# Kernel tuning notes

Hardware: AMD Instinct MI355X
Metric: run time of the kernel (lower is better)

## Reference

```python
import jax, jax.numpy as jnp
import numpy as np

EPS = 1e-08
N_NODES = 100000
D = 128
N_EDGES = 3200000


def _gcn_conv(x, w, b, edge_index, n):
    # PyG GCNConv: add self-loops, symmetric deg^{-1/2} normalization,
    # out = scatter_add(norm * (x @ w)[src] -> dst) + bias
    loops = jnp.arange(n, dtype=edge_index.dtype)
    src = jnp.concatenate([edge_index[0], loops])
    dst = jnp.concatenate([edge_index[1], loops])
    deg = jax.ops.segment_sum(jnp.ones_like(dst, dtype=x.dtype), dst, num_segments=n)
    dinv = jnp.where(deg > 0, jax.lax.rsqrt(deg), 0.0)
    norm = dinv[src] * dinv[dst]                      # [E+N]
    h = x @ w                                          # [N, D]
    msg = h[src] * norm[:, None]                       # [E+N, D] (dominant traffic)
    return jax.ops.segment_sum(msg, dst, num_segments=n) + b


def setup_inputs() -> dict:
    key = jax.random.key(0)
    ks = jax.random.split(key, 8)
    s = 1.0 / np.sqrt(D)
    return {
        "edge_index": jax.random.randint(ks[0], (2, N_EDGES), 0, N_NODES, dtype=jnp.int64),
        "eps": jax.random.normal(ks[1], (N_NODES, D), dtype=jnp.float32),
        "vrepr": jax.random.normal(ks[2], (N_NODES, D), dtype=jnp.float32) * 0.02,
        "conv_w": jax.random.uniform(ks[3], (D, D), jnp.float32, -s, s),
        "conv_b": jnp.zeros((D,), jnp.float32),
        "loc_w": jax.random.uniform(ks[4], (D, D), jnp.float32, -s, s),
        "loc_b": jax.random.uniform(ks[5], (D,), jnp.float32, -s, s),
        "std_w": jax.random.uniform(ks[6], (D, D), jnp.float32, -s, s),
        "std_b": jax.random.uniform(ks[7], (D,), jnp.float32, -s, s),
    }


def reference(edge_index, eps, vrepr, conv_w, conv_b, loc_w, loc_b, std_w, std_b):
    n = vrepr.shape[0]
    h = _gcn_conv(vrepr, conv_w, conv_b, edge_index, n)   # [N, D]
    loc = h @ loc_w.T + loc_b
    std = jax.nn.softplus(h @ std_w.T + std_b) + EPS
    logvar = jnp.log(std ** 2)
    z = loc + std * eps                                    # Normal(loc, std).rsample()
    return (z, loc, logvar)
```

## Files before the change

### kernel.cpp

```cpp
#include <hip/hip_runtime.h>
#include <math.h>


typedef short short8 __attribute__((ext_vector_type(8)));
typedef float f32x4 __attribute__((ext_vector_type(4)));

#define NT 64
#define MAXCELL 1568
#define CPT 7
#define CHUNK 8192
#define CHUNKC 32768
#define CAPB 4096
#define BPB 256
#define RPT (CAPB / BPB)
#define FBLK 768

static __device__ __forceinline__ unsigned short f2bf(float x) {
  unsigned u = __float_as_uint(x);
  unsigned r = (u + 0x7fffu + ((u >> 16) & 1u)) >> 16;
  return (unsigned short)r;
}


#if __has_builtin(__builtin_amdgcn_cvt_f32_fp8)
static __device__ __forceinline__ float fp8dec(unsigned v, int sel) {
  switch (sel) {
    case 0: return __builtin_amdgcn_cvt_f32_fp8((int)v, 0);
    case 1: return __builtin_amdgcn_cvt_f32_fp8((int)v, 1);
    case 2: return __builtin_amdgcn_cvt_f32_fp8((int)v, 2);
    default: return __builtin_amdgcn_cvt_f32_fp8((int)v, 3);
  }
}
#else
static __device__ __forceinline__ float fp8dec1(unsigned b) {
  unsigned s = b >> 7, e = (b >> 3) & 15, m = b & 7;
  float mag = e ? __uint_as_float(((e + 120u) << 23) | (m << 20))
                : (float)m * 0.001953125f;
  return s ? -mag : mag;
}
static __device__ __forceinline__ float fp8dec(unsigned v, int sel) {
  return fp8dec1((v >> (8 * sel)) & 0xff);
}
#endif

static __device__ __forceinline__ unsigned fp8enc(float v) {
#if __has_builtin(__builtin_amdgcn_cvt_pk_fp8_f32)
  return (unsigned)__builtin_amdgcn_cvt_pk_fp8_f32(v, 0.0f, 0, false) & 0xffu;
#else
  unsigned u = __float_as_uint(v);
  unsigned s = (u >> 24) & 0x80u;
  int e = (int)((u >> 23) & 0xff) - 127;
  unsigned m = u & 0x7fffffu;
  if (e < -9) return s;
  if (e >= 9) return s | 0x7e;
  if (e >= -6) {
    unsigned keep = m >> 20;
    unsigned rem = m & 0xfffffu;
    keep += (rem > 0x80000u) || (rem == 0x80000u && (keep & 1));
    unsigned ee = (unsigned)(e + 7);
    if (keep == 8) { keep = 0; ee += 1; if (ee >= 16) return s | 0x7e; }
    return s | (ee << 3) | keep;
  }
  float q = fabsf(v) * 512.0f;
  unsigned k = (unsigned)(q + 0.5f);
  if (k >= 8) return s | 0x08;
  return s | k;
#endif
}

static __device__ void block_scan_cells(int* cnt, int* off, int* scanT, int ncell, int tid)
{
  int c0 = tid * CPT;
  int lsum = 0;
#pragma unroll
  for (int u = 0; u < CPT; ++u) { int c = c0 + u; if (c < ncell) lsum += cnt[c]; }
  scanT[tid] = lsum;
  __syncthreads();
  for (int o = 1; o < 256; o <<= 1) {
    int add = (tid >= o) ? scanT[tid - o] : 0;
    __syncthreads();
    scanT[tid] += add;
    __syncthreads();
  }
  int run = scanT[tid] - lsum;
#pragma unroll
  for (int u = 0; u < CPT; ++u) {
    int c = c0 + u;
    if (c < ncell) { off[c] = run; run += cnt[c]; }
  }
}

__global__ void k_zero_int(int* __restrict__ p, int n) {
  int i = blockIdx.x * blockDim.x + threadIdx.x;
  if (i < n) p[i] = 0;
}


__global__ __launch_bounds__(512)
void k_cellcnt(const int4* __restrict__ dst4, int* __restrict__ cellCnt, int nE4, int ncell)
{
  __shared__ int h[MAXCELL];
  const int tid = threadIdx.x;
  const int base4 = blockIdx.x * (CHUNKC / 4);
  for (int i = tid; i < ncell; i += 512) h[i] = 0;
  __syncthreads();
#pragma unroll
  for (int k = 0; k < CHUNKC / 4 / 512; ++k) {
    int i4 = base4 + tid + k * 512;
    if (i4 < nE4) {
      int4 d = dst4[i4];
      atomicAdd(&h[d.x >> 6], 1);
      atomicAdd(&h[d.y >> 6], 1);
      atomicAdd(&h[d.z >> 6], 1);
      atomicAdd(&h[d.w >> 6], 1);
    }
  }
  __syncthreads();
  for (int i = tid; i < ncell; i += 512) if (h[i]) atomicAdd(&cellCnt[i], h[i]);
}


__global__ __launch_bounds__(256)
void k_cellscan(const int* __restrict__ cellCnt, int* __restrict__ gOff,
                int* __restrict__ gCur, int ncell)
{
  __shared__ int c[MAXCELL], o[MAXCELL], scanT[256];
  const int tid = threadIdx.x;
  for (int i = tid; i < ncell; i += 256) c[i] = cellCnt[i];
  __syncthreads();
  block_scan_cells(c, o, scanT, ncell, tid);
  __syncthreads();
  for (int i = tid; i < ncell; i += 256) { gOff[i] = o[i]; gCur[i] = o[i]; }
}


__global__ __launch_bounds__(256)
void k_passA(const int4* __restrict__ src4, const int4* __restrict__ dst4,
             int* __restrict__ gCur, unsigned* __restrict__ gEdges, int nE4, int ncell)
{
  __shared__ unsigned stagePk[CHUNK];
  __shared__ unsigned short stageCell[CHUNK];
  __shared__ int cntA[MAXCELL], offA[MAXCELL], curA[MAXCELL], scanT[256];
  const int tid = threadIdx.x;
  const int base4 = blockIdx.x * (CHUNK / 4);
  const int C = min(CHUNK, nE4 * 4 - base4 * 4);

  for (int i = tid; i < ncell; i += 256) cntA[i] = 0;
  __syncthreads();
#pragma unroll
  for (int k = 0; k < CHUNK / 4 / 256; ++k) {
    int i4 = base4 + tid + k * 256;
    if (i4 < nE4) {
      int4 d = dst4[i4];
      atomicAdd(&cntA[d.x >> 6], 1);
      atomicAdd(&cntA[d.y >> 6], 1);
      atomicAdd(&cntA[d.z >> 6], 1);
      atomicAdd(&cntA[d.w >> 6], 1);
    }
  }
  __syncthreads();
  block_scan_cells(cntA, offA, scanT, ncell, tid);
  __syncthreads();
  for (int i = tid; i < ncell; i += 256) curA[i] = offA[i];
  __syncthreads();
#pragma unroll
  for (int k = 0; k < CHUNK / 4 / 256; ++k) {
    int i4 = base4 + tid + k * 256;
    if (i4 < nE4) {
      int4 d = dst4[i4];
      int4 s = src4[i4];
#pragma unroll
      for (int u = 0; u < 4; ++u) {
        int dd = (u == 0) ? d.x : (u == 1) ? d.y : (u == 2) ? d.z : d.w;
        int ss = (u == 0) ? s.x : (u == 1) ? s.y : (u == 2) ? s.z : s.w;
        int c = dd >> 6, dl = dd & 63;
        int pos = atomicAdd(&curA[c], 1);
        stagePk[pos] = (unsigned)ss | ((unsigned)dl << 17);
        stageCell[pos] = (unsigned short)c;
      }
    }
  }
  __syncthreads();
  for (int i = tid; i < ncell; i += 256) {
    int cv = cntA[i];
    if (cv > 0) {
      int b = atomicAdd(&gCur[i], cv);
      cntA[i] = b - offA[i];
    }
  }
  __syncthreads();
#pragma unroll
  for (int k = 0; k < CHUNK / 256; ++k) {
    int p = tid + k * 256;
    if (p < C) {
      int c = stageCell[p];
      gEdges[cntA[c] + p] = stagePk[p];
    }
  }
}


__global__ __launch_bounds__(256)
void k_cnt_dinv(const unsigned* __restrict__ gEdges, const int* __restrict__ gOff,
                const int* __restrict__ cellCnt, float* __restrict__ dinv, int n)
{
  __shared__ int cnt[NT];
  const int c = blockIdx.x, tid = threadIdx.x;
  if (tid < NT) cnt[tid] = 0;
  __syncthreads();
  const int off = gOff[c], m = cellCnt[c];
  for (int i = tid; i < m; i += 256) atomicAdd(&cnt[gEdges[off + i] >> 17], 1);
  __syncthreads();
  int d = c * NT + tid;
  if (tid < NT && d < n) dinv[d] = rsqrtf((float)cnt[tid] + 1.0f);
}


__global__ void k_vs(const float* __restrict__ vrepr, const float* __restrict__ dinv,
                     unsigned* __restrict__ vs, int n)
{
  int i = blockIdx.x * 256 + threadIdx.x;
  if (i >= n * 32) return;
  int row = i >> 5;
  float4 v = ((const float4*)vrepr)[i];
  float dd = dinv[row] * 128.0f;
#if __has_builtin(__builtin_amdgcn_cvt_pk_fp8_f32)
  int w = __builtin_amdgcn_cvt_pk_fp8_f32(v.x * dd, v.y * dd, 0, false);
  w = __builtin_amdgcn_cvt_pk_fp8_f32(v.z * dd, v.w * dd, w, true);
  vs[i] = (unsigned)w;
#else
  vs[i] = fp8enc(v.x * dd) | (fp8enc(v.y * dd) << 8) |
          (fp8enc(v.z * dd) << 16) | (fp8enc(v.w * dd) << 24);
#endif
}


__global__ __launch_bounds__(128)
void k_wcomb(const float* __restrict__ cw, const float* __restrict__ cb,
             const float* __restrict__ hw, const float* __restrict__ hb,
             unsigned short* __restrict__ wt, float* __restrict__ bout)
{
  int j = blockIdx.x, k = threadIdx.x;
  __shared__ float s[128];
  s[k] = hw[j * 128 + k];
  __syncthreads();
  float acc = 0.f;
  const float* r = cw + k * 128;
#pragma unroll 8
  for (int m = 0; m < 128; ++m) acc = fmaf(r[m], s[m], acc);
  wt[j * 128 + k] = f2bf(acc);
  if (k == 0) {
    float b = 0.f;
    for (int m = 0; m < 128; ++m) b = fmaf(cb[m], s[m], b);
    bout[j] = b + hb[j];
  }
}


__global__ __launch_bounds__(BPB)
void k_passB(const unsigned* __restrict__ gEdges, const int* __restrict__ gOff,
             const int* __restrict__ cellCnt, const float* __restrict__ dinv,
             const unsigned* __restrict__ vs32, float* __restrict__ hagg, int n)
{
  __shared__ unsigned sortedE[CAPB];
  __shared__ int hist[NT];
  __shared__ int segOff[NT + 1];
  const int c = blockIdx.x, tid = threadIdx.x;
  const int d0 = c * NT;
  const int off0 = gOff[c], m = cellCnt[c];
  const int wv = tid >> 6, lane = tid & 63;
  const int half = lane >> 5;
  const int l32 = lane & 31;

  const int nchunk = m > 0 ? (m + CAPB - 1) / CAPB : 1;
  for (int ch = 0; ch < nchunk; ++ch) {
    const int cb = ch * CAPB;
    const int mc = min(CAPB, m - cb) > 0 ? min(CAPB, m - cb) : 0;

    if (ch > 0) __syncthreads();
    for (int i = tid; i < NT; i += BPB) hist[i] = 0;
    __syncthreads();

    unsigned rawE[RPT];
#pragma unroll
    for (int k = 0; k < RPT; ++k) {
      int i = tid + k * BPB;
      unsigned pk = 0xffffffffu;
      if (i < mc) {
        pk = gEdges[off0 + cb + i];
        atomicAdd(&hist[pk >> 17], 1);
      }
      rawE[k] = pk;
    }
    __syncthreads();
    if (tid == 0) {
      int run = 0;
      for (int r = 0; r < NT; ++r) { segOff[r] = run; run += hist[r]; }
      segOff[NT] = run;
    }
    __syncthreads();
    for (int i = tid; i < NT; i += BPB) hist[i] = segOff[i];
    __syncthreads();
#pragma unroll
    for (int k = 0; k < RPT; ++k) {
      unsigned pk = rawE[k];
      if (pk != 0xffffffffu)
        sortedE[atomicAdd(&hist[pk >> 17], 1)] = pk;
    }
    __syncthreads();

    for (int r = wv; r < NT; r += 4) {
      int d = d0 + r;
      if (d >= n) continue;
      float a0 = 0.f, a1 = 0.f, a2 = 0.f, a3 = 0.f;
      int i = segOff[r];
      const int e = segOff[r + 1];
      for (; i + 16 <= e; i += 16) {
#pragma unroll
        for (int j = 0; j < 8; ++j) {
          unsigned pk = sortedE[i + 2 * j + half];
          unsigned v = vs32[(size_t)(pk & 0x1FFFF) * 32 + l32];
          a0 += fp8dec(v, 0); a1 += fp8dec(v, 1);
          a2 += fp8dec(v, 2); a3 += fp8dec(v, 3);
        }
      }
      for (; i + 2 <= e; i += 2) {
        unsigned pk = sortedE[i + half];
        unsigned v = vs32[(size_t)(pk & 0x1FFFF) * 32 + l32];
        a0 += fp8dec(v, 0); a1 += fp8dec(v, 1);
        a2 += fp8dec(v, 2); a3 += fp8dec(v, 3);
      }
      if (i < e && half == 0) {
        unsigned pk = sortedE[i];
        unsigned v = vs32[(size_t)(pk & 0x1FFFF) * 32 + l32];
        a0 += fp8dec(v, 0); a1 += fp8dec(v, 1);
        a2 += fp8dec(v, 2); a3 += fp8dec(v, 3);
      }
      a0 += __shfl_xor(a0, 32);
      a1 += __shfl_xor(a1, 32);
      a2 += __shfl_xor(a2, 32);
      a3 += __shfl_xor(a3, 32);

      if (half == 0) {
        const float dd = dinv[d] * 0.0078125f;
        float4 out;
        if (ch == 0) {
          unsigned sp = vs32[(size_t)d * 32 + l32];
          out = make_float4((a0 + fp8dec(sp, 0)) * dd, (a1 + fp8dec(sp, 1)) * dd,
                            (a2 + fp8dec(sp, 2)) * dd, (a3 + fp8dec(sp, 3)) * dd);
        } else {
          float4 prev = ((const float4*)hagg)[(size_t)d * 32 + l32];
          out = make_float4(prev.x + a0 * dd, prev.y + a1 * dd,
                            prev.z + a2 * dd, prev.w + a3 * dd);
        }
        ((float4*)hagg)[(size_t)d * 32 + l32] = out;
      }
    }
  }
}


#define LPAD 132

__global__ __launch_bounds__(512)
void k_fused(const float* hagg,
             const unsigned short* __restrict__ wlT, const unsigned short* __restrict__ wsT,
             const float* __restrict__ bl, const float* __restrict__ bs,
             const float* __restrict__ eps,
             float* __restrict__ z, float* loc, float* __restrict__ lv,
             int n, int ntiles)
{
  __shared__ float sLoc[32 * LPAD];
  __shared__ float sStd[32 * LPAD];
  const int t = threadIdx.x;
  const int w = t >> 6;
  const int L = t & 63;
  const int rg = (w >> 2) * 16;
  const int c0 = (w & 3) * 32;
  const int lr = L & 15;
  const int lk = L >> 4;

  short8 bw[2][2][4];
  float blv[2], bsv[2];
#pragma unroll
  for (int head = 0; head < 2; ++head) {
    const unsigned short* W = head ? wsT : wlT;
#pragma unroll
    for (int ct = 0; ct < 2; ++ct) {
      int col = c0 + ct * 16 + lr;
#pragma unroll
      for (int kt = 0; kt < 4; ++kt)
        bw[head][ct][kt] = *(const short8*)(W + col * 128 + kt * 32 + lk * 8);
    }
  }
#pragma unroll
  for (int ct = 0; ct < 2; ++ct) {
    blv[ct] = bl[c0 + ct * 16 + lr];
    bsv[ct] = bs[c0 + ct * 16 + lr];
  }

  for (int tile = blockIdx.x; tile < ntiles; tile += gridDim.x) {
    const int rbase = tile * 32 + rg;
    const int arow = min(rbase + lr, n - 1);

    short8 a[4];
#pragma unroll
    for (int kt = 0; kt < 4; ++kt) {
      const float* p = hagg + (size_t)arow * 128 + kt * 32 + lk * 8;
      float4 f0 = *(const float4*)p;
      float4 f1 = *(const float4*)(p + 4);
      short8 v;
      v[0] = f2bf(f0.x); v[1] = f2bf(f0.y); v[2] = f2bf(f0.z); v[3] = f2bf(f0.w);
      v[4] = f2bf(f1.x); v[5] = f2bf(f1.y); v[6] = f2bf(f1.z); v[7] = f2bf(f1.w);
      a[kt] = v;
    }

    f32x4 accL[2], accS[2];
#pragma unroll
    for (int ct = 0; ct < 2; ++ct) { accL[ct] = (f32x4)0.f; accS[ct] = (f32x4)0.f; }
#pragma unroll
    for (int kt = 0; kt < 4; ++kt) {
      accL[0] = __builtin_amdgcn_mfma_f32_16x16x32_bf16(a[kt], bw[0][0][kt], accL[0], 0, 0, 0);
      accL[1] = __builtin_amdgcn_mfma_f32_16x16x32_bf16(a[kt], bw[0][1][kt], accL[1], 0, 0, 0);
      accS[0] = __builtin_amdgcn_mfma_f32_16x16x32_bf16(a[kt], bw[1][0][kt], accS[0], 0, 0, 0);
      accS[1] = __builtin_amdgcn_mfma_f32_16x16x32_bf16(a[kt], bw[1][1][kt], accS[1], 0, 0, 0);
    }

#pragma unroll
    for (int ct = 0; ct < 2; ++ct) {
      int col = c0 + ct * 16 + lr;
#pragma unroll
      for (int reg = 0; reg < 4; ++reg) {
        int rl = rg + lk * 4 + reg;
        sLoc[rl * LPAD + col] = accL[ct][reg] + blv[ct];
        sStd[rl * LPAD + col] = accS[ct][reg] + bsv[ct];
      }
    }
    __syncthreads();

    const int blk0 = tile * 32;
#pragma unroll
    for (int i = t; i < 1024; i += 512) {
      int rl = i >> 5, c4 = i & 31;
      int row = blk0 + rl;
      if (row < n) {
        float4 lcv = *(const float4*)&sLoc[rl * LPAD + c4 * 4];
        float4 srv = *(const float4*)&sStd[rl * LPAD + c4 * 4];
        size_t o4 = (size_t)row * 32 + c4;
        float4 e4 = ((const float4*)eps)[o4];
        float4 zv, lvv, svv;
        {
          float s0 = fmaxf(srv.x, 0.f) + __logf(1.f + __expf(-fabsf(srv.x))) + 1e-8f;
          float s1 = fmaxf(srv.y, 0.f) + __logf(1.f + __expf(-fabsf(srv.y))) + 1e-8f;
          float s2 = fmaxf(srv.z, 0.f) + __logf(1.f + __expf(-fabsf(srv.z))) + 1e-8f;
          float s3 = fmaxf(srv.w, 0.f) + __logf(1.f + __expf(-fabsf(srv.w))) + 1e-8f;
          svv = make_float4(s0, s1, s2, s3);
        }
        zv.x = fmaf(svv.x, e4.x, lcv.x); zv.y = fmaf(svv.y, e4.y, lcv.y);
        zv.z = fmaf(svv.z, e4.z, lcv.z); zv.w = fmaf(svv.w, e4.w, lcv.w);
        lvv.x = 2.f * __logf(svv.x); lvv.y = 2.f * __logf(svv.y);
        lvv.z = 2.f * __logf(svv.z); lvv.w = 2.f * __logf(svv.w);
        ((float4*)z)[o4] = zv;
        ((float4*)loc)[o4] = lcv;
        ((float4*)lv)[o4] = lvv;
      }
    }
    __syncthreads();
  }
}

extern "C" void kernel_launch(void* const* d_in, const int* in_sizes, int n_in,
                              void* d_out, int out_size, void* d_ws, size_t ws_size,
                              hipStream_t stream)
{
  const int*   edge   = (const int*)d_in[0];
  const float* eps    = (const float*)d_in[1];
  const float* vrepr  = (const float*)d_in[2];
  const float* conv_w = (const float*)d_in[3];
  const float* conv_b = (const float*)d_in[4];
  const float* loc_w  = (const float*)d_in[5];
  const float* loc_b  = (const float*)d_in[6];
  const float* std_w  = (const float*)d_in[7];
  const float* std_b  = (const float*)d_in[8];

  const int nE = in_sizes[0] / 2;
  const int n  = in_sizes[1] / 128;
  const size_t ND = (size_t)n * 128;
  const int ncell = (n + NT - 1) / NT;
  const int nE4 = nE / 4;

  float*          dinv = (float*)d_ws;
  unsigned short* wlT  = (unsigned short*)(dinv + n);
  unsigned short* wsT  = wlT + 16384;
  float*          bl   = (float*)(wsT + 16384);
  float*          bs   = bl + 128;

  float* r0 = (float*)d_out;
  float* r1 = r0 + ND;
  float* r2 = r1 + ND;

  unsigned* vs = (unsigned*)r0;

  unsigned* gEdges  = (unsigned*)r2;
  int*      cellCnt = (int*)(gEdges + nE);
  int*      gOff    = cellCnt + ncell;
  int*      gCur    = gOff + ncell;

  const int* srcIdx = edge;
  const int* dstIdx = edge + nE;

  k_zero_int<<<(ncell + 255) / 256, 256, 0, stream>>>(cellCnt, ncell);
  k_cellcnt<<<(nE + CHUNKC - 1) / CHUNKC, 512, 0, stream>>>(
      (const int4*)dstIdx, cellCnt, nE4, ncell);
  k_cellscan<<<1, 256, 0, stream>>>(cellCnt, gOff, gCur, ncell);
  k_passA<<<(nE + CHUNK - 1) / CHUNK, 256, 0, stream>>>(
      (const int4*)srcIdx, (const int4*)dstIdx, gCur, gEdges, nE4, ncell);
  k_cnt_dinv<<<ncell, 256, 0, stream>>>(gEdges, gOff, cellCnt, dinv, n);

  k_vs<<<(n * 32 + 255) / 256, 256, 0, stream>>>(vrepr, dinv, vs, n);
  k_wcomb<<<128, 128, 0, stream>>>(conv_w, conv_b, loc_w, loc_b, wlT, bl);
  k_wcomb<<<128, 128, 0, stream>>>(conv_w, conv_b, std_w, std_b, wsT, bs);

  k_passB<<<ncell, BPB, 0, stream>>>(gEdges, gOff, cellCnt, dinv, vs, r1, n);

  const int ntiles = (n + 31) / 32;
  k_fused<<<FBLK, 512, 0, stream>>>(r1, wlT, wsT, bl, bs, eps, r0, r1, r2, n, ntiles);
}
```

Before: 227.9 us.

## Store aggregated features as bf16, merge weight-combine launches, prefetch eps early

```diff
diff --git a/kernel.cpp b/kernel.cpp
--- a/kernel.cpp
+++ b/kernel.cpp
@@ -19,6 +19,9 @@
   unsigned u = __float_as_uint(x);
   unsigned r = (u + 0x7fffu + ((u >> 16) & 1u)) >> 16;
   return (unsigned short)r;
+}
+static __device__ __forceinline__ float bf2f(unsigned short u) {
+  return __uint_as_float((unsigned)u << 16);
 }
 
 
@@ -236,11 +239,17 @@
 
 
 __global__ __launch_bounds__(128)
-void k_wcomb(const float* __restrict__ cw, const float* __restrict__ cb,
-             const float* __restrict__ hw, const float* __restrict__ hb,
-             unsigned short* __restrict__ wt, float* __restrict__ bout)
-{
-  int j = blockIdx.x, k = threadIdx.x;
+void k_wcomb2(const float* __restrict__ cw, const float* __restrict__ cb,
+              const float* __restrict__ lw, const float* __restrict__ lb,
+              const float* __restrict__ sw, const float* __restrict__ sb,
+              unsigned short* __restrict__ wlT, unsigned short* __restrict__ wsT,
+              float* __restrict__ bl, float* __restrict__ bs)
+{
+  const int head = blockIdx.x >> 7, j = blockIdx.x & 127, k = threadIdx.x;
+  const float* hw = head ? sw : lw;
+  const float* hb = head ? sb : lb;
+  unsigned short* wt = head ? wsT : wlT;
+  float* bout = head ? bs : bl;
   __shared__ float s[128];
   s[k] = hw[j * 128 + k];
   __syncthreads();
@@ -257,10 +266,12 @@
 }
 
 
+template <int BF16H>
 __global__ __launch_bounds__(BPB)
 void k_passB(const unsigned* __restrict__ gEdges, const int* __restrict__ gOff,
              const int* __restrict__ cellCnt, const float* __restrict__ dinv,
-             const unsigned* __restrict__ vs32, float* __restrict__ hagg, int n)
+             const unsigned* __restrict__ vs32, float* __restrict__ hagg,
+             unsigned short* __restrict__ hagg16, int n)
 {
   __shared__ unsigned sortedE[CAPB];
   __shared__ int hist[NT];
@@ -348,12 +359,23 @@
           unsigned sp = vs32[(size_t)d * 32 + l32];
           out = make_float4((a0 + fp8dec(sp, 0)) * dd, (a1 + fp8dec(sp, 1)) * dd,
                             (a2 + fp8dec(sp, 2)) * dd, (a3 + fp8dec(sp, 3)) * dd);
+        } else if (BF16H) {
+          ushort4 pv = *(const ushort4*)(hagg16 + (size_t)d * 128 + 4 * l32);
+          out = make_float4(bf2f(pv.x) + a0 * dd, bf2f(pv.y) + a1 * dd,
+                            bf2f(pv.z) + a2 * dd, bf2f(pv.w) + a3 * dd);
         } else {
           float4 prev = ((const float4*)hagg)[(size_t)d * 32 + l32];
           out = make_float4(prev.x + a0 * dd, prev.y + a1 * dd,
                             prev.z + a2 * dd, prev.w + a3 * dd);
         }
-        ((float4*)hagg)[(size_t)d * 32 + l32] = out;
+        if (BF16H) {
+          ushort4 o;
+          o.x = f2bf(out.x); o.y = f2bf(out.y);
+          o.z = f2bf(out.z); o.w = f2bf(out.w);
+          *(ushort4*)(hagg16 + (size_t)d * 128 + 4 * l32) = o;
+        } else {
+          ((float4*)hagg)[(size_t)d * 32 + l32] = out;
+        }
       }
     }
   }
@@ -362,8 +384,10 @@
 
 #define LPAD 132
 
+template <int BF16H>
 __global__ __launch_bounds__(512)
 void k_fused(const float* hagg,
+             const unsigned short* __restrict__ hagg16,
              const unsigned short* __restrict__ wlT, const unsigned short* __restrict__ wsT,
              const float* __restrict__ bl, const float* __restrict__ bs,
              const float* __restrict__ eps,
@@ -399,6 +423,8 @@
     bsv[ct] = bs[c0 + ct * 16 + lr];
   }
 
+  const int rlA = t >> 5, c4e = t & 31;
+
   for (int tile = blockIdx.x; tile < ntiles; tile += gridDim.x) {
     const int rbase = tile * 32 + rg;
     const int arow = min(rbase + lr, n - 1);
@@ -406,14 +432,23 @@
     short8 a[4];
 #pragma unroll
     for (int kt = 0; kt < 4; ++kt) {
-      const float* p = hagg + (size_t)arow * 128 + kt * 32 + lk * 8;
-      float4 f0 = *(const float4*)p;
-      float4 f1 = *(const float4*)(p + 4);
-      short8 v;
-      v[0] = f2bf(f0.x); v[1] = f2bf(f0.y); v[2] = f2bf(f0.z); v[3] = f2bf(f0.w);
-      v[4] = f2bf(f1.x); v[5] = f2bf(f1.y); v[6] = f2bf(f1.z); v[7] = f2bf(f1.w);
-      a[kt] = v;
-    }
+      if (BF16H) {
+        a[kt] = *(const short8*)(hagg16 + (size_t)arow * 128 + kt * 32 + lk * 8);
+      } else {
+        const float* p = hagg + (size_t)arow * 128 + kt * 32 + lk * 8;
+        float4 f0 = *(const float4*)p;
+        float4 f1 = *(const float4*)(p + 4);
+        short8 v;
+        v[0] = f2bf(f0.x); v[1] = f2bf(f0.y); v[2] = f2bf(f0.z); v[3] = f2bf(f0.w);
+        v[4] = f2bf(f1.x); v[5] = f2bf(f1.y); v[6] = f2bf(f1.z); v[7] = f2bf(f1.w);
+        a[kt] = v;
+      }
+    }
+
+    const int blk0 = tile * 32;
+    const int rowA = blk0 + rlA, rowB = rowA + 16;
+    float4 e4a = ((const float4*)eps)[(size_t)min(rowA, n - 1) * 32 + c4e];
+    float4 e4b = ((const float4*)eps)[(size_t)min(rowB, n - 1) * 32 + c4e];
 
     f32x4 accL[2], accS[2];
 #pragma unroll
@@ -438,16 +473,15 @@
     }
     __syncthreads();
 
-    const int blk0 = tile * 32;
-#pragma unroll
-    for (int i = t; i < 1024; i += 512) {
-      int rl = i >> 5, c4 = i & 31;
-      int row = blk0 + rl;
+#pragma unroll
+    for (int u = 0; u < 2; ++u) {
+      const int rl = rlA + u * 16;
+      const int row = u ? rowB : rowA;
       if (row < n) {
-        float4 lcv = *(const float4*)&sLoc[rl * LPAD + c4 * 4];
-        float4 srv = *(const float4*)&sStd[rl * LPAD + c4 * 4];
-        size_t o4 = (size_t)row * 32 + c4;
-        float4 e4 = ((const float4*)eps)[o4];
+        float4 lcv = *(const float4*)&sLoc[rl * LPAD + c4e * 4];
+        float4 srv = *(const float4*)&sStd[rl * LPAD + c4e * 4];
+        float4 e4 = u ? e4b : e4a;
+        size_t o4 = (size_t)row * 32 + c4e;
         float4 zv, lvv, svv;
         {
           float s0 = fmaxf(srv.x, 0.f) + __logf(1.f + __expf(-fabsf(srv.x))) + 1e-8f;
@@ -489,11 +523,15 @@
   const int ncell = (n + NT - 1) / NT;
   const int nE4 = nE / 4;
 
-  float*          dinv = (float*)d_ws;
-  unsigned short* wlT  = (unsigned short*)(dinv + n);
-  unsigned short* wsT  = wlT + 16384;
-  float*          bl   = (float*)(wsT + 16384);
-  float*          bs   = bl + 128;
+  float*          dinv   = (float*)d_ws;
+  unsigned short* wlT    = (unsigned short*)(dinv + n);
+  unsigned short* wsT    = wlT + 16384;
+  float*          bl     = (float*)(wsT + 16384);
+  float*          bs     = bl + 128;
+  unsigned short* hagg16 = (unsigned short*)(bs + 128);
+
+  const size_t need = (size_t)((char*)(hagg16 + ND) - (char*)d_ws);
+  const bool big_ws = ws_size >= need;
 
   float* r0 = (float*)d_out;
   float* r1 = r0 + ND;
@@ -518,11 +556,19 @@
   k_cnt_dinv<<<ncell, 256, 0, stream>>>(gEdges, gOff, cellCnt, dinv, n);
 
   k_vs<<<(n * 32 + 255) / 256, 256, 0, stream>>>(vrepr, dinv, vs, n);
-  k_wcomb<<<128, 128, 0, stream>>>(conv_w, conv_b, loc_w, loc_b, wlT, bl);
-  k_wcomb<<<128, 128, 0, stream>>>(conv_w, conv_b, std_w, std_b, wsT, bs);
-
-  k_passB<<<ncell, BPB, 0, stream>>>(gEdges, gOff, cellCnt, dinv, vs, r1, n);
+  k_wcomb2<<<256, 128, 0, stream>>>(conv_w, conv_b, loc_w, loc_b, std_w, std_b,
+                                    wlT, wsT, bl, bs);
 
   const int ntiles = (n + 31) / 32;
-  k_fused<<<FBLK, 512, 0, stream>>>(r1, wlT, wsT, bl, bs, eps, r0, r1, r2, n, ntiles);
-}
+  if (big_ws) {
+    k_passB<1><<<ncell, BPB, 0, stream>>>(gEdges, gOff, cellCnt, dinv, vs,
+                                          r1, hagg16, n);
+    k_fused<1><<<FBLK, 512, 0, stream>>>(r1, hagg16, wlT, wsT, bl, bs, eps,
+                                         r0, r1, r2, n, ntiles);
+  } else {
+    k_passB<0><<<ncell, BPB, 0, stream>>>(gEdges, gOff, cellCnt, dinv, vs,
+                                          r1, hagg16, n);
+    k_fused<0><<<FBLK, 512, 0, stream>>>(r1, hagg16, wlT, wsT, bl, bs, eps,
+                                         r0, r1, r2, n, ntiles);
+  }
+}
```

Measured after the change: 218.5 us. -4.1%, faster.
